# Kernel optimization log

Hardware: AMD Instinct MI355X
Metric: run time of the kernel (lower is better)

Reference implementation:

```python
import jax, jax.numpy as jnp
import numpy as np

H, D, K = 8, 512, 64
EPS = 1e-12


def _l2norm(x):
    # F.normalize(p=2, dim=-1): x / max(||x||_2, eps)
    n = jnp.sqrt(jnp.sum(x * x, axis=-1, keepdims=True))
    return x / jnp.maximum(n, EPS)


def setup_inputs() -> dict:
    key = jax.random.key(0)
    ks = jax.random.split(key, 8)
    S, B = 1024, 16
    scale = 1.0 / np.sqrt(D)
    return {
        "query": jax.random.normal(ks[0], (S, B, D), dtype=jnp.float32),
        "key": jax.random.normal(ks[1], (S, B, D), dtype=jnp.float32),
        "value": jax.random.normal(ks[2], (S, B, D), dtype=jnp.float32),
        # stacked per-head projection weights, torch Linear convention [out,in]
        "WQ": jax.random.uniform(ks[3], (H, K, D), jnp.float32, -scale, scale),
        "WK": jax.random.uniform(ks[4], (H, K, D), jnp.float32, -scale, scale),
        "WV": jax.random.uniform(ks[5], (H, K, D), jnp.float32, -scale, scale),
        "Wout": jax.random.uniform(ks[6], (D, H * K), jnp.float32,
                                   -1.0 / np.sqrt(H * K), 1.0 / np.sqrt(H * K)),
    }


def reference(query, key, value, WQ, WK, WV, Wout):
    temp = K ** 0.5
    # project all heads at once: [S,B,D] x [H,K,D] -> [B,H,S,K]
    wq = _l2norm(jnp.einsum("sbd,hkd->bhsk", query, WQ))
    wk = _l2norm(jnp.einsum("sbd,hkd->bhsk", key, WK))
    wv = _l2norm(jnp.einsum("sbd,hkd->bhsk", value, WV))
    # cosine-similarity attention scores [B,H,Sq,Sk]
    scores = jnp.einsum("bhsk,bhtk->bhst", wq, wk) / temp
    aff = jax.nn.softmax(scores, axis=-1)
    out = jnp.einsum("bhst,bhtk->bhsk", aff, wv)  # [B,H,S,K]
    # concat heads -> [S,B,H*K] (matches torch per-head concat on last dim)
    Sq, B = query.shape[0], query.shape[1]
    concat = out.transpose(2, 0, 1, 3).reshape(Sq, B, H * K)
    return concat @ Wout.T  # [S,B,D]
```

## Files before the change

### kernel.cpp

```cpp
#include <hip/hip_runtime.h>
#include <cstdint>
#include <cstddef>

typedef unsigned int u32;
typedef unsigned short u16;
typedef __attribute__((ext_vector_type(8))) short short8;
typedef __attribute__((ext_vector_type(4))) float f32x4;

#define S_LEN 1024
#define BATCH 16
#define NHEAD 8
#define DMODEL 512
#define KHD 64
#define NROW (S_LEN * BATCH)

__device__ __forceinline__ u16 f2bf(float f) {
    u32 u = __float_as_uint(f);
    return (u16)((u + 0x7fffu + ((u >> 16) & 1u)) >> 16);
}

__device__ __forceinline__ void gl_lds16(const void* g, void* l) {
    __builtin_amdgcn_global_load_lds(
        (const __attribute__((address_space(1))) void*)(uintptr_t)g,
        (__attribute__((address_space(3))) void*)(uintptr_t)l, 16, 0, 0);
}

__global__ __launch_bounds__(256) void wcvt_kernel(
    const float* __restrict__ WQ, const float* __restrict__ WK,
    const float* __restrict__ WV, const float* __restrict__ Wo,
    u16* __restrict__ dst)
{
    const int m = blockIdx.y;
    const float* __restrict__ src = (m == 0) ? WQ : (m == 1) ? WK : (m == 2) ? WV : Wo;
    const int idx = (blockIdx.x * 256 + threadIdx.x) * 4;
    const float4 v = *(const float4*)(src + idx);
    u16 r[4];
    r[0] = f2bf(v.x); r[1] = f2bf(v.y); r[2] = f2bf(v.z); r[3] = f2bf(v.w);
    *(uint2*)(dst + (size_t)m * DMODEL * DMODEL + idx) = *(uint2*)r;
}

__global__ __launch_bounds__(256) void xcvt_kernel(
    const float* __restrict__ s0, const float* __restrict__ s1,
    u16* __restrict__ dst)
{
    const float* __restrict__ src = (blockIdx.y == 0) ? s0 : s1;
    u16* d = dst + (size_t)blockIdx.y * NROW * DMODEL;
    const int idx = (blockIdx.x * 256 + threadIdx.x) * 4;
    const float4 v = *(const float4*)(src + idx);
    u16 r[4];
    r[0] = f2bf(v.x); r[1] = f2bf(v.y); r[2] = f2bf(v.z); r[3] = f2bf(v.w);
    *(uint2*)(d + idx) = *(uint2*)r;
}

template<int M>
__global__ __launch_bounds__(256) void gemm_kernel(
    const u16* __restrict__ Abf,
    const u16* __restrict__ Wb,
    u16* __restrict__ outN,
    float* __restrict__ outP)
{
    __shared__ __align__(16) u16 Alds[128 * 64];
    __shared__ __align__(16) u16 Blds[128 * 64];

    const int tid  = threadIdx.x;
    const int wave = tid >> 6;
    const int lane = tid & 63;
    const int m16  = lane & 15;
    const int quad = lane >> 4;
    const int wm   = wave >> 1;
    const int wn   = wave & 1;
    const int n0   = blockIdx.y * 128;
    const int row0 = blockIdx.x * 128;
    const int z    = (M == 1) ? blockIdx.z : 0;
    const int bb   = (M == 2) ? blockIdx.z : 0;

    const u16* __restrict__ A = Abf + (size_t)z * NROW * DMODEL + (size_t)bb * DMODEL;
    const size_t astr = (M == 2) ? (size_t)BATCH * DMODEL : (size_t)DMODEL;
    const u16* __restrict__ B = Wb + ((M == 1) ? (size_t)z * DMODEL * DMODEL : 0);

    f32x4 acc[4][4] = {};

    const int brow   = lane >> 3;
    const int bchunk = (lane & 7) ^ brow;

    for (int kt = 0; kt < DMODEL; kt += 64) {
        __syncthreads();
        {
            const u16* ap = A + (size_t)(row0 + wave * 32 + brow) * astr + kt + bchunk * 8;
            const u16* bp = B + (size_t)(n0 + wave * 32 + brow) * DMODEL + kt + bchunk * 8;
            u16* la = &Alds[(wave * 32) * 64];
            u16* lb = &Blds[(wave * 32) * 64];
#pragma unroll
            for (int j = 0; j < 4; j++) {
                gl_lds16(ap + (size_t)j * 8 * astr,   la + j * 8 * 64);
                gl_lds16(bp + (size_t)j * 8 * DMODEL, lb + j * 8 * 64);
            }
        }
        __syncthreads();

#pragma unroll
        for (int half = 0; half < 2; half++) {
            short8 af[4], bfr[4];
#pragma unroll
            for (int mt = 0; mt < 4; mt++)
                af[mt] = *(const short8*)&Alds[(wm * 64 + mt * 16 + m16) * 64 +
                                               (((half << 2) + quad) ^ (m16 & 7)) * 8];
#pragma unroll
            for (int nt = 0; nt < 4; nt++)
                bfr[nt] = *(const short8*)&Blds[(wn * 64 + nt * 16 + m16) * 64 +
                                                (((half << 2) + quad) ^ (m16 & 7)) * 8];
#pragma unroll
            for (int mt = 0; mt < 4; mt++)
#pragma unroll
                for (int nt = 0; nt < 4; nt++)
                    acc[mt][nt] = __builtin_amdgcn_mfma_f32_16x16x32_bf16(af[mt], bfr[nt], acc[mt][nt], 0, 0, 0);
        }
    }

    if (M == 1) {
        const int h = (n0 >> 6) + wn;
        u16* outZ = outN + (size_t)z * BATCH * NHEAD * S_LEN * KHD;
#pragma unroll
        for (int mt = 0; mt < 4; mt++) {
#pragma unroll
            for (int r = 0; r < 4; r++) {
                float ss = 0.0f;
#pragma unroll
                for (int nt = 0; nt < 4; nt++) ss += acc[mt][nt][r] * acc[mt][nt][r];
                ss += __shfl_xor(ss, 1);
                ss += __shfl_xor(ss, 2);
                ss += __shfl_xor(ss, 4);
                ss += __shfl_xor(ss, 8);
                const float sc = 1.0f / fmaxf(sqrtf(ss), 1e-12f);
                const int i = row0 + wm * 64 + mt * 16 + quad * 4 + r;
                const int s = i >> 4, b = i & 15;
                u16* op = outZ + (((size_t)b * NHEAD + h) * S_LEN + s) * KHD;
#pragma unroll
                for (int nt = 0; nt < 4; nt++)
                    op[nt * 16 + m16] = f2bf(acc[mt][nt][r] * sc);
            }
        }
    } else if (M == 2) {
        const int h = (n0 >> 6) + wn;
#pragma unroll
        for (int mt = 0; mt < 4; mt++) {
            float scl[4];
#pragma unroll
            for (int r = 0; r < 4; r++) {
                float ss = 0.0f;
#pragma unroll
                for (int nt = 0; nt < 4; nt++) ss += acc[mt][nt][r] * acc[mt][nt][r];
                ss += __shfl_xor(ss, 1);
                ss += __shfl_xor(ss, 2);
                ss += __shfl_xor(ss, 4);
                ss += __shfl_xor(ss, 8);
                scl[r] = 1.0f / fmaxf(sqrtf(ss), 1e-12f);
            }
            const int sbase = row0 + wm * 64 + mt * 16 + quad * 4;
#pragma unroll
            for (int nt = 0; nt < 4; nt++) {
                const int vcol = nt * 16 + m16;
                uint2 pk;
                pk.x = (u32)f2bf(acc[mt][nt][0] * scl[0]) |
                       ((u32)f2bf(acc[mt][nt][1] * scl[1]) << 16);
                pk.y = (u32)f2bf(acc[mt][nt][2] * scl[2]) |
                       ((u32)f2bf(acc[mt][nt][3] * scl[3]) << 16);
                u16* dp = outN + (((size_t)bb * NHEAD + h) * KHD + vcol) * S_LEN + sbase;
                *(uint2*)dp = pk;
            }
        }
    } else {
#pragma unroll
        for (int mt = 0; mt < 4; mt++) {
#pragma unroll
            for (int r = 0; r < 4; r++) {
                const int i = row0 + wm * 64 + mt * 16 + quad * 4 + r;
                float* op = outP + (size_t)i * DMODEL + n0 + wn * 64;
#pragma unroll
                for (int nt = 0; nt < 4; nt++)
                    op[nt * 16 + m16] = acc[mt][nt][r];
            }
        }
    }
}

__global__ __launch_bounds__(256) void attn_kernel(
    const u16* __restrict__ wq, const u16* __restrict__ wk, const u16* __restrict__ wvT,
    u16* __restrict__ Xc)
{
    __shared__ __align__(16) u16 Klds[64 * 64];
    __shared__ __align__(16) u16 Vlds[64 * 64];
    __shared__ __align__(16) u16 Plds[4][16 * 72];

    const int tid  = threadIdx.x;
    const int wave = tid >> 6;
    const int lane = tid & 63;
    const int m16  = lane & 15;
    const int quad = lane >> 4;
    const int qt   = blockIdx.x;
    const int bh   = blockIdx.y;

    const u16* Qb = wq  + (size_t)bh * S_LEN * KHD;
    const u16* Kb = wk  + (size_t)bh * S_LEN * KHD;
    const u16* Vb = wvT + (size_t)bh * KHD * S_LEN;

    const int qrow = qt * 64 + wave * 16 + m16;
    const short8 qf0 = *(const short8*)(Qb + (size_t)qrow * KHD + quad * 8);
    const short8 qf1 = *(const short8*)(Qb + (size_t)qrow * KHD + 32 + quad * 8);

    short8 ones;
#pragma unroll
    for (int j = 0; j < 8; j++) ones[j] = (short)0x3F80;

    f32x4 o[4] = {};
    f32x4 ls  = {};
    const float C1 = 0.125f, C2 = 0.0078125f, C3 = 3.2552083e-4f;

    const int srow   = lane >> 3;
    const int schunk = (lane & 7) ^ srow;

    for (int it = 0; it < S_LEN / 64; it++) {
        const int kt0 = it * 64;
        __syncthreads();
        {
            const int r0 = wave * 8 + srow;
            gl_lds16(Kb + (size_t)(kt0 + r0) * KHD + schunk * 8,        &Klds[(wave * 8) * 64]);
            gl_lds16(Kb + (size_t)(kt0 + r0 + 32) * KHD + schunk * 8,   &Klds[(wave * 8 + 32) * 64]);
            gl_lds16(Vb + (size_t)r0 * S_LEN + kt0 + schunk * 8,        &Vlds[(wave * 8) * 64]);
            gl_lds16(Vb + (size_t)(r0 + 32) * S_LEN + kt0 + schunk * 8, &Vlds[(wave * 8 + 32) * 64]);
        }
        __syncthreads();

#pragma unroll
        for (int mt = 0; mt < 4; mt++) {
            const short8 kf0 = *(const short8*)&Klds[(mt * 16 + m16) * 64 + (quad ^ (m16 & 7)) * 8];
            const short8 kf1 = *(const short8*)&Klds[(mt * 16 + m16) * 64 + ((4 + quad) ^ (m16 & 7)) * 8];
            f32x4 c = {};
            c = __builtin_amdgcn_mfma_f32_16x16x32_bf16(kf0, qf0, c, 0, 0, 0);
            c = __builtin_amdgcn_mfma_f32_16x16x32_bf16(kf1, qf1, c, 0, 0, 0);
            u32 up[4];
#pragma unroll
            for (int r = 0; r < 4; r++) {
                const float y = c[r];
                const float p = fmaf(fmaf(fmaf(C3, y, C2), y, C1), y, 1.0f);
                up[r] = __float_as_uint(p);
            }
            uint2 pk;
            pk.x = (up[0] >> 16) | (up[1] & 0xffff0000u);
            pk.y = (up[2] >> 16) | (up[3] & 0xffff0000u);
            *(uint2*)&Plds[wave][m16 * 72 + mt * 16 + quad * 4] = pk;
        }

#pragma unroll
        for (int c = 0; c < 2; c++) {
            const short8 pb = *(const short8*)&Plds[wave][m16 * 72 + c * 32 + quad * 8];
            ls = __builtin_amdgcn_mfma_f32_16x16x32_bf16(ones, pb, ls, 0, 0, 0);
#pragma unroll
            for (int vt = 0; vt < 4; vt++) {
                const short8 vf = *(const short8*)&Vlds[(vt * 16 + m16) * 64 +
                                                        (((c << 2) + quad) ^ (m16 & 7)) * 8];
                o[vt] = __builtin_amdgcn_mfma_f32_16x16x32_bf16(vf, pb, o[vt], 0, 0, 0);
            }
        }
    }

    const float inv = 1.0f / ls[0];
    const int b = bh >> 3, h = bh & 7;
    u16* cp = Xc + ((size_t)qrow * BATCH + b) * (NHEAD * KHD) + h * KHD;
#pragma unroll
    for (int vt = 0; vt < 4; vt++) {
        uint2 pk;
        pk.x = (u32)f2bf(o[vt][0] * inv) | ((u32)f2bf(o[vt][1] * inv) << 16);
        pk.y = (u32)f2bf(o[vt][2] * inv) | ((u32)f2bf(o[vt][3] * inv) << 16);
        *(uint2*)(cp + vt * 16 + quad * 4) = pk;
    }
}

extern "C" void kernel_launch(void* const* d_in, const int* in_sizes, int n_in,
                              void* d_out, int out_size, void* d_ws, size_t ws_size,
                              hipStream_t stream) {
    const float* q    = (const float*)d_in[0];
    const float* k    = (const float*)d_in[1];
    const float* v    = (const float*)d_in[2];
    const float* WQ   = (const float*)d_in[3];
    const float* WK   = (const float*)d_in[4];
    const float* WV   = (const float*)d_in[5];
    const float* Wout = (const float*)d_in[6];
    float* out = (float*)d_out;
    u16*  Xbf = (u16*)d_out;

    const size_t per = (size_t)BATCH * NHEAD * S_LEN * KHD;
    u16* wsQKV = (u16*)d_ws;
    u16* wsW   = wsQKV + 3 * per;

    wcvt_kernel<<<dim3(256, 4), 256, 0, stream>>>(WQ, WK, WV, Wout, wsW);

    xcvt_kernel<<<dim3(NROW * DMODEL / 1024, 2), 256, 0, stream>>>(q, k, Xbf);

    gemm_kernel<1><<<dim3(NROW / 128, DMODEL / 128, 2), 256, 0, stream>>>(
        Xbf, wsW, wsQKV, nullptr);

    xcvt_kernel<<<dim3(NROW * DMODEL / 1024, 1), 256, 0, stream>>>(v, v, Xbf);

    gemm_kernel<2><<<dim3(S_LEN / 128, DMODEL / 128, BATCH), 256, 0, stream>>>(
        Xbf, wsW + (size_t)2 * DMODEL * DMODEL, wsQKV + 2 * per, nullptr);

    attn_kernel<<<dim3(S_LEN / 64, BATCH * NHEAD), 256, 0, stream>>>(
        wsQKV, wsQKV + per, wsQKV + 2 * per, Xbf);

    hipMemcpyAsync(wsQKV, Xbf, (size_t)NROW * DMODEL * sizeof(u16),
                   hipMemcpyDeviceToDevice, stream);

    gemm_kernel<0><<<dim3(NROW / 128, DMODEL / 128, 1), 256, 0, stream>>>(
        wsQKV, wsW + (size_t)3 * DMODEL * DMODEL, nullptr, out);
}
```

Measured before the change: 280.4 us.

## Double-buffer K/V tiles in attention, swizzle P buffer, reorder grid

The attention kernel now keeps two LDS buffers for K and V and issues async global-to-LDS loads for the next tile before computing on the current one, so there is one barrier per iteration instead of two. The P staging buffer drops its padded stride in favour of an XOR swizzle, which shrinks LDS use and is meant to avoid bank conflicts. It also raises wave priority around the PV MFMA section and swaps grid dimensions so blocks of the same head run close together for L2 reuse. LDS use doubles for K/V, which may lower occupancy, and correctness relies on the single barrier at the end of each loop iteration.

```diff
diff --git a/kernel.cpp b/kernel.cpp
--- a/kernel.cpp
+++ b/kernel.cpp
@@ -188,17 +188,17 @@
     const u16* __restrict__ wq, const u16* __restrict__ wk, const u16* __restrict__ wvT,
     u16* __restrict__ Xc)
 {
-    __shared__ __align__(16) u16 Klds[64 * 64];
-    __shared__ __align__(16) u16 Vlds[64 * 64];
-    __shared__ __align__(16) u16 Plds[4][16 * 72];
+    __shared__ __align__(16) u16 Klds[2][64 * 64];
+    __shared__ __align__(16) u16 Vlds[2][64 * 64];
+    __shared__ __align__(16) u16 Plds[4][16 * 64];
 
     const int tid  = threadIdx.x;
     const int wave = tid >> 6;
     const int lane = tid & 63;
     const int m16  = lane & 15;
     const int quad = lane >> 4;
-    const int qt   = blockIdx.x;
-    const int bh   = blockIdx.y;
+    const int bh   = blockIdx.x;
+    const int qt   = blockIdx.y;
 
     const u16* Qb = wq  + (size_t)bh * S_LEN * KHD;
     const u16* Kb = wk  + (size_t)bh * S_LEN * KHD;
@@ -218,23 +218,30 @@
 
     const int srow   = lane >> 3;
     const int schunk = (lane & 7) ^ srow;
+    const int r0     = wave * 8 + srow;
+
+    gl_lds16(Kb + (size_t)r0 * KHD + schunk * 8,               &Klds[0][(wave * 8) * 64]);
+    gl_lds16(Kb + (size_t)(r0 + 32) * KHD + schunk * 8,        &Klds[0][(wave * 8 + 32) * 64]);
+    gl_lds16(Vb + (size_t)r0 * S_LEN + schunk * 8,             &Vlds[0][(wave * 8) * 64]);
+    gl_lds16(Vb + (size_t)(r0 + 32) * S_LEN + schunk * 8,      &Vlds[0][(wave * 8 + 32) * 64]);
+    __syncthreads();
 
     for (int it = 0; it < S_LEN / 64; it++) {
-        const int kt0 = it * 64;
-        __syncthreads();
-        {
-            const int r0 = wave * 8 + srow;
-            gl_lds16(Kb + (size_t)(kt0 + r0) * KHD + schunk * 8,        &Klds[(wave * 8) * 64]);
-            gl_lds16(Kb + (size_t)(kt0 + r0 + 32) * KHD + schunk * 8,   &Klds[(wave * 8 + 32) * 64]);
-            gl_lds16(Vb + (size_t)r0 * S_LEN + kt0 + schunk * 8,        &Vlds[(wave * 8) * 64]);
-            gl_lds16(Vb + (size_t)(r0 + 32) * S_LEN + kt0 + schunk * 8, &Vlds[(wave * 8 + 32) * 64]);
-        }
-        __syncthreads();
+        const int cur = it & 1;
+
+        if (it + 1 < S_LEN / 64) {
+            const int nxt = cur ^ 1;
+            const int kt0 = (it + 1) * 64;
+            gl_lds16(Kb + (size_t)(kt0 + r0) * KHD + schunk * 8,        &Klds[nxt][(wave * 8) * 64]);
+            gl_lds16(Kb + (size_t)(kt0 + r0 + 32) * KHD + schunk * 8,   &Klds[nxt][(wave * 8 + 32) * 64]);
+            gl_lds16(Vb + (size_t)r0 * S_LEN + kt0 + schunk * 8,        &Vlds[nxt][(wave * 8) * 64]);
+            gl_lds16(Vb + (size_t)(r0 + 32) * S_LEN + kt0 + schunk * 8, &Vlds[nxt][(wave * 8 + 32) * 64]);
+        }
 
 #pragma unroll
         for (int mt = 0; mt < 4; mt++) {
-            const short8 kf0 = *(const short8*)&Klds[(mt * 16 + m16) * 64 + (quad ^ (m16 & 7)) * 8];
-            const short8 kf1 = *(const short8*)&Klds[(mt * 16 + m16) * 64 + ((4 + quad) ^ (m16 & 7)) * 8];
+            const short8 kf0 = *(const short8*)&Klds[cur][(mt * 16 + m16) * 64 + (quad ^ (m16 & 7)) * 8];
+            const short8 kf1 = *(const short8*)&Klds[cur][(mt * 16 + m16) * 64 + ((4 + quad) ^ (m16 & 7)) * 8];
             f32x4 c = {};
             c = __builtin_amdgcn_mfma_f32_16x16x32_bf16(kf0, qf0, c, 0, 0, 0);
             c = __builtin_amdgcn_mfma_f32_16x16x32_bf16(kf1, qf1, c, 0, 0, 0);
@@ -248,20 +255,27 @@
             uint2 pk;
             pk.x = (up[0] >> 16) | (up[1] & 0xffff0000u);
             pk.y = (up[2] >> 16) | (up[3] & 0xffff0000u);
-            *(uint2*)&Plds[wave][m16 * 72 + mt * 16 + quad * 4] = pk;
-        }
-
+            u16* pwp = (u16*)((char*)Plds[wave] + m16 * 128 +
+                              ((((mt << 1) + (quad >> 1)) ^ (m16 & 7)) << 4) + ((quad & 1) << 3));
+            *(uint2*)pwp = pk;
+        }
+
+        __builtin_amdgcn_s_setprio(1);
 #pragma unroll
         for (int c = 0; c < 2; c++) {
-            const short8 pb = *(const short8*)&Plds[wave][m16 * 72 + c * 32 + quad * 8];
+            const short8 pb = *(const short8*)((const char*)Plds[wave] + m16 * 128 +
+                                               (((c * 4 + quad) ^ (m16 & 7)) << 4));
             ls = __builtin_amdgcn_mfma_f32_16x16x32_bf16(ones, pb, ls, 0, 0, 0);
 #pragma unroll
             for (int vt = 0; vt < 4; vt++) {
-                const short8 vf = *(const short8*)&Vlds[(vt * 16 + m16) * 64 +
-                                                        (((c << 2) + quad) ^ (m16 & 7)) * 8];
+                const short8 vf = *(const short8*)&Vlds[cur][(vt * 16 + m16) * 64 +
+                                                             (((c << 2) + quad) ^ (m16 & 7)) * 8];
                 o[vt] = __builtin_amdgcn_mfma_f32_16x16x32_bf16(vf, pb, o[vt], 0, 0, 0);
             }
         }
+        __builtin_amdgcn_s_setprio(0);
+
+        __syncthreads();
     }
 
     const float inv = 1.0f / ls[0];
@@ -305,7 +319,7 @@
     gemm_kernel<2><<<dim3(S_LEN / 128, DMODEL / 128, BATCH), 256, 0, stream>>>(
         Xbf, wsW + (size_t)2 * DMODEL * DMODEL, wsQKV + 2 * per, nullptr);
 
-    attn_kernel<<<dim3(S_LEN / 64, BATCH * NHEAD), 256, 0, stream>>>(
+    attn_kernel<<<dim3(BATCH * NHEAD, S_LEN / 64), 256, 0, stream>>>(
         wsQKV, wsQKV + per, wsQKV + 2 * per, Xbf);
 
     hipMemcpyAsync(wsQKV, Xbf, (size_t)NROW * DMODEL * sizeof(u16),
```

Measured after the change: 274.4 us. 1.02x faster.
